# Optimization experiments

Hardware: AMD Instinct MI355X
Metric: run time of the kernel (lower is better)

The kernel has to match this reference:

```python
import jax, jax.numpy as jnp
import numpy as np

N_NODES = 100000
N_EDGES = 1200000
IN_DIM = 64
HID = 64
OUT = 10
N_GRAPHS = 256


def setup_inputs() -> dict:
    key = jax.random.key(0)
    ks = jax.random.split(key, 10)
    x = jax.random.normal(ks[0], (N_NODES, IN_DIM), dtype=jnp.float32)
    edge_index = jax.random.randint(ks[1], (2, N_EDGES), 0, N_NODES, dtype=jnp.int64)
    batch = jnp.sort(jax.random.randint(ks[2], (N_NODES,), 0, N_GRAPHS, dtype=jnp.int64))
    # GCNConv weights (glorot) and biases, final linear
    def glorot(k, fan_in, fan_out):
        s = jnp.sqrt(6.0 / (fan_in + fan_out)).astype(jnp.float32)
        return jax.random.uniform(k, (fan_in, fan_out), jnp.float32, -s, s)
    W1 = glorot(ks[3], IN_DIM, HID)
    b1 = jnp.zeros((HID,), jnp.float32)
    W2 = glorot(ks[4], HID, HID)
    b2 = jnp.zeros((HID,), jnp.float32)
    Wl = glorot(ks[5], HID, OUT)
    bl = jnp.zeros((OUT,), jnp.float32)
    return {"x": x, "edge_index": edge_index, "batch": batch,
            "W1": W1, "b1": b1, "W2": W2, "b2": b2, "Wl": Wl, "bl": bl}


def _gcn_conv(x, W, b, src, dst, n):
    # PyG GCNConv: add self-loops, symmetric deg^-1/2 normalization,
    # transform then aggregate, plus bias.
    h = x @ W  # [N, F_out]
    loop = jnp.arange(n, dtype=src.dtype)
    src_f = jnp.concatenate([src, loop])
    dst_f = jnp.concatenate([dst, loop])
    deg = jax.ops.segment_sum(jnp.ones_like(dst_f, dtype=h.dtype), dst_f, num_segments=n)
    dinv = jax.lax.rsqrt(jnp.maximum(deg, 1.0))  # self-loops guarantee deg>=1
    norm = dinv[src_f] * dinv[dst_f]  # [E+N]
    msgs = h[src_f] * norm[:, None]   # gather + scale (memory-bound)
    agg = jax.ops.segment_sum(msgs, dst_f, num_segments=n)
    return agg + b


def reference(x, edge_index, batch, W1, b1, W2, b2, Wl, bl):
    n = x.shape[0]
    src, dst = edge_index[0], edge_index[1]
    h = jax.nn.relu(_gcn_conv(x, W1, b1, src, dst, n))
    h = jax.nn.relu(_gcn_conv(h, W2, b2, src, dst, n))
    # global_mean_pool over batch vector
    sums = jax.ops.segment_sum(h, batch, num_segments=N_GRAPHS)
    cnt = jax.ops.segment_sum(jnp.ones((n,), h.dtype), batch, num_segments=N_GRAPHS)
    pooled = sums / jnp.maximum(cnt, 1.0)[:, None]  # [G, HID]
    return pooled @ Wl + bl  # [G, OUT]
```

## Files before the change

kernel.cpp:

```cpp
#include <hip/hip_runtime.h>
#include <hip/hip_bf16.h>


#define NFEAT 64
#define CAP 40

__device__ __forceinline__ float bf2f(__hip_bfloat16 h) { return __bfloat162float(h); }

__global__ __launch_bounds__(256) void dinv_kernel(const int* __restrict__ cursor,
                                                   float* __restrict__ dinv, int n) {
    int i = blockIdx.x * blockDim.x + threadIdx.x;
    if (i < n) dinv[i] = rsqrtf((float)(cursor[i] + 1));
}

__device__ __forceinline__ void gemm_rows(const float* __restrict__ in,
                                          __hip_bfloat16* __restrict__ out,
                                          int nRows, int rowBlock,
                                          float* wl, float* xrow) {
    const int tid = threadIdx.x;
    const int lane = tid & 63;
    const int w = tid >> 6;
    const int base = rowBlock * 64 + w * 16;
    for (int i = 0; i < 16; i++) {
        int r = base + i;
        if (r >= nRows) break;
        xrow[w * 64 + lane] = in[(size_t)r * NFEAT + lane];
        float acc = 0.f;
        const float4* x4 = (const float4*)(xrow + w * 64);
        #pragma unroll
        for (int kk = 0; kk < 16; kk++) {
            float4 xv = x4[kk];
            acc = fmaf(xv.x, wl[(kk * 4 + 0) * 64 + lane], acc);
            acc = fmaf(xv.y, wl[(kk * 4 + 1) * 64 + lane], acc);
            acc = fmaf(xv.z, wl[(kk * 4 + 2) * 64 + lane], acc);
            acc = fmaf(xv.w, wl[(kk * 4 + 3) * 64 + lane], acc);
        }
        out[(size_t)r * NFEAT + lane] = __float2bfloat16(acc);
    }
}

__global__ __launch_bounds__(256) void scatter_gemm1(
        const float* __restrict__ x, const float* __restrict__ W1,
        __hip_bfloat16* __restrict__ hbuf, int nN,
        const int* __restrict__ src, const int* __restrict__ dst,
        int* __restrict__ cursor, int* __restrict__ pad, int nE,
        int nGemmBlk, int edgesPerRank, int rng) {
    __shared__ float wl[64 * 64];
    __shared__ float xrow[4 * 64];
    const int b = blockIdx.x;
    if (b < nGemmBlk) {
        const int tid = threadIdx.x;
        #pragma unroll
        for (int i = 0; i < 16; i++) wl[tid + i * 256] = W1[tid + i * 256];
        __syncthreads();
        gemm_rows(x, hbuf, nN, b, wl, xrow);
    } else {
        const int xcd = b & 7;
        const int rank = (b - nGemmBlk) >> 3;
        const int lo = xcd * rng;
        int e0 = rank * edgesPerRank;
        int e1 = e0 + edgesPerRank; if (e1 > nE) e1 = nE;
        for (int e = e0 + threadIdx.x; e < e1; e += 256) {
            int d = dst[e];
            if ((unsigned)(d - lo) < (unsigned)rng) {
                int pos = atomicAdd(&cursor[d], 1);
                if (pos < CAP) pad[(size_t)d * CAP + pos] = src[e];
            }
        }
    }
}

__device__ __forceinline__ float agg_node(const __hip_bfloat16* __restrict__ hs,
                                          const float* __restrict__ dinv,
                                          const int* __restrict__ cursor,
                                          const int* __restrict__ pad,
                                          int n, int lane) {
    int cnt = cursor[n];
    cnt = cnt < CAP ? cnt : CAP;
    const float dn = dinv[n];
    const int* row = pad + (size_t)n * CAP;
    float acc = bf2f(hs[(size_t)n * NFEAT + lane]) * dn;
    int i = 0;
    for (; i + 3 < cnt; i += 4) {
        int s0 = row[i], s1 = row[i + 1], s2 = row[i + 2], s3 = row[i + 3];
        float d0 = dinv[s0], d1 = dinv[s1], d2 = dinv[s2], d3 = dinv[s3];
        float v0 = bf2f(hs[(size_t)s0 * NFEAT + lane]);
        float v1 = bf2f(hs[(size_t)s1 * NFEAT + lane]);
        float v2 = bf2f(hs[(size_t)s2 * NFEAT + lane]);
        float v3 = bf2f(hs[(size_t)s3 * NFEAT + lane]);
        acc = fmaf(v0, d0, acc); acc = fmaf(v1, d1, acc);
        acc = fmaf(v2, d2, acc); acc = fmaf(v3, d3, acc);
    }
    for (; i < cnt; ++i) {
        int s = row[i];
        acc = fmaf(bf2f(hs[(size_t)s * NFEAT + lane]), dinv[s], acc);
    }
    return acc * dn;
}

__global__ __launch_bounds__(256) void aggL1_gemm2(
        const __hip_bfloat16* __restrict__ hs1, const float* __restrict__ dinv,
        const int* __restrict__ cursor, const int* __restrict__ pad,
        const float* __restrict__ W2, const float* __restrict__ b1,
        __hip_bfloat16* __restrict__ hs2, int nN) {
    __shared__ float wl[64 * 64];
    __shared__ float xrow[4 * 64];
    const int tid = threadIdx.x;
    const int lane = tid & 63;
    const int w = tid >> 6;
    #pragma unroll
    for (int i = 0; i < 16; i++) wl[tid + i * 256] = W2[tid + i * 256];
    const float blane = b1[lane];
    __syncthreads();

    const int base = blockIdx.x * 16 + w * 4;
    #pragma unroll
    for (int i = 0; i < 4; i++) {
        int n = base + i;
        if (n >= nN) break;
        float a = agg_node(hs1, dinv, cursor, pad, n, lane);
        xrow[w * 64 + lane] = fmaxf(a + blane, 0.f);
        float acc = 0.f;
        const float4* x4 = (const float4*)(xrow + w * 64);
        #pragma unroll
        for (int kk = 0; kk < 16; kk++) {
            float4 xv = x4[kk];
            acc = fmaf(xv.x, wl[(kk * 4 + 0) * 64 + lane], acc);
            acc = fmaf(xv.y, wl[(kk * 4 + 1) * 64 + lane], acc);
            acc = fmaf(xv.z, wl[(kk * 4 + 2) * 64 + lane], acc);
            acc = fmaf(xv.w, wl[(kk * 4 + 3) * 64 + lane], acc);
        }
        hs2[(size_t)n * NFEAT + lane] = __float2bfloat16(acc);
    }
}

__global__ __launch_bounds__(256) void aggL2_pool(
        const __hip_bfloat16* __restrict__ hs2, const float* __restrict__ dinv,
        const int* __restrict__ cursor, const int* __restrict__ pad,
        const float* __restrict__ b2, const int* __restrict__ batch,
        float* __restrict__ psum, int nN) {
    const int lane = threadIdx.x & 63;
    const int w = threadIdx.x >> 6;
    const int n0 = (blockIdx.x * 4 + w) * 4;
    if (n0 >= nN) return;
    const int nEnd = (n0 + 4 < nN) ? n0 + 4 : nN;
    const float b = b2[lane];
    int gprev = batch[n0];
    float pacc = 0.f;
    for (int n = n0; n < nEnd; ++n) {
        int g = batch[n];
        if (g != gprev) {
            unsafeAtomicAdd(&psum[(size_t)gprev * NFEAT + lane], pacc);
            pacc = 0.f;
            gprev = g;
        }
        float a = agg_node(hs2, dinv, cursor, pad, n, lane);
        pacc += fmaxf(a + b, 0.f);
    }
    unsafeAtomicAdd(&psum[(size_t)gprev * NFEAT + lane], pacc);
}

__global__ __launch_bounds__(64) void final_kernel(const float* __restrict__ psum,
                                                   const int* __restrict__ batch, int nN,
                                                   const float* __restrict__ Wl,
                                                   const float* __restrict__ bl,
                                                   float* __restrict__ out) {
    const int g = blockIdx.x;
    const int j = threadIdx.x;
    int lo = 0, hi = nN;
    while (lo < hi) { int mid = (lo + hi) >> 1; if (batch[mid] < g) lo = mid + 1; else hi = mid; }
    const int start = lo;
    hi = nN;
    while (lo < hi) { int mid = (lo + hi) >> 1; if (batch[mid] < g + 1) lo = mid + 1; else hi = mid; }
    const int cnt = lo - start;
    __shared__ float p[64];
    p[j] = psum[g * 64 + j] / (float)(cnt > 1 ? cnt : 1);
    __syncthreads();
    if (j < 10) {
        float acc = bl[j];
        #pragma unroll
        for (int f = 0; f < 64; f++) acc = fmaf(p[f], Wl[f * 10 + j], acc);
        out[g * 10 + j] = acc;
    }
}

static inline size_t align256(size_t s) { return (s + 255) & ~(size_t)255; }

extern "C" void kernel_launch(void* const* d_in, const int* in_sizes, int n_in,
                              void* d_out, int out_size, void* d_ws, size_t ws_size,
                              hipStream_t stream) {
    const float* x     = (const float*)d_in[0];
    const int*   ei    = (const int*)d_in[1];
    const int*   batch = (const int*)d_in[2];
    const float* W1    = (const float*)d_in[3];
    const float* b1    = (const float*)d_in[4];
    const float* W2    = (const float*)d_in[5];
    const float* b2    = (const float*)d_in[6];
    const float* Wl    = (const float*)d_in[7];
    const float* bl    = (const float*)d_in[8];
    float* out = (float*)d_out;

    const int nN = in_sizes[0] / NFEAT;
    const int nE = in_sizes[1] / 2;
    const int nG = 256;
    const int* src = ei;
    const int* dst = ei + nE;

    char* w = (char*)d_ws;
    float* dinv   = (float*)w; w += align256((size_t)nN * 4);
    int*   cursor = (int*)w;   w += align256((size_t)nN * 4);
    int*   pad    = (int*)w;   w += align256((size_t)nN * CAP * 4);
    __hip_bfloat16* hs1 = (__hip_bfloat16*)w; w += align256((size_t)nN * NFEAT * 2);
    __hip_bfloat16* hs2 = (__hip_bfloat16*)w; w += align256((size_t)nN * NFEAT * 2);
    float* psum   = (float*)w; w += align256((size_t)nG * NFEAT * 4);

    const int nBlkN   = (nN + 255) / 256;
    const int nBlkRow = (nN + 63) / 64;
    const int nBlkAgg = (nN + 15) / 16;
    const int nGemmBlk = (nBlkRow + 7) & ~7;
    const int ranksPerXcd = 586;
    const int nScatBlk = ranksPerXcd * 8;
    const int edgesPerRank = (nE + ranksPerXcd - 1) / ranksPerXcd;
    const int rng = (nN + 7) / 8;

    (void)hipMemsetAsync(cursor, 0, (size_t)nN * 4, stream);
    (void)hipMemsetAsync(psum, 0, (size_t)nG * NFEAT * 4, stream);

    scatter_gemm1<<<nGemmBlk + nScatBlk, 256, 0, stream>>>(
        x, W1, hs1, nN, src, dst, cursor, pad, nE, nGemmBlk, edgesPerRank, rng);
    dinv_kernel<<<nBlkN, 256, 0, stream>>>(cursor, dinv, nN);

    aggL1_gemm2<<<nBlkAgg, 256, 0, stream>>>(hs1, dinv, cursor, pad, W2, b1, hs2, nN);

    aggL2_pool<<<nBlkAgg, 256, 0, stream>>>(hs2, dinv, cursor, pad, b2, batch, psum, nN);

    final_kernel<<<nG, 64, 0, stream>>>(psum, batch, nN, Wl, bl, out);
}
```

Baseline: 221.1 us.

## Prescale features by dinv, gather bf16 pairs with half-wave edge split

Replaces the separate dinv kernel with a pass that computes dinv and pre-multiplies the layer-1 bf16 features by the source node's dinv. Layer 2 features are likewise scaled at store time, so the aggregation loops need no per-neighbor dinv gathers. Each lane now loads two packed bf16 values, and the two half-waves split the neighbor list between them before being combined with a shuffle. The scatter stage also moves from 8 destination ranges to 4. Pre-scaling adds an extra read-modify-write pass over hs1 and rounds the scaled values to bf16 a second time.

Result: no change. 221.4 us (+0.2%).

```diff
diff --git a/kernel.cpp b/kernel.cpp
--- a/kernel.cpp
+++ b/kernel.cpp
@@ -5,13 +5,10 @@
 #define NFEAT 64
 #define CAP 40
 
-__device__ __forceinline__ float bf2f(__hip_bfloat16 h) { return __bfloat162float(h); }
-
-__global__ __launch_bounds__(256) void dinv_kernel(const int* __restrict__ cursor,
-                                                   float* __restrict__ dinv, int n) {
-    int i = blockIdx.x * blockDim.x + threadIdx.x;
-    if (i < n) dinv[i] = rsqrtf((float)(cursor[i] + 1));
-}
+typedef unsigned int uint;
+
+__device__ __forceinline__ float bflo(uint v) { return __uint_as_float(v << 16); }
+__device__ __forceinline__ float bfhi(uint v) { return __uint_as_float(v & 0xffff0000u); }
 
 __device__ __forceinline__ void gemm_rows(const float* __restrict__ in,
                                           __hip_bfloat16* __restrict__ out,
@@ -55,9 +52,9 @@
         __syncthreads();
         gemm_rows(x, hbuf, nN, b, wl, xrow);
     } else {
-        const int xcd = b & 7;
-        const int rank = (b - nGemmBlk) >> 3;
-        const int lo = xcd * rng;
+        const int range = (b & 7) >> 1;
+        const int rank = ((b - nGemmBlk) >> 3) * 2 + (b & 1);
+        const int lo = range * rng;
         int e0 = rank * edgesPerRank;
         int e1 = e0 + edgesPerRank; if (e1 > nE) e1 = nE;
         for (int e = e0 + threadIdx.x; e < e1; e += 256) {
@@ -70,36 +67,63 @@
     }
 }
 
-__device__ __forceinline__ float agg_node(const __hip_bfloat16* __restrict__ hs,
-                                          const float* __restrict__ dinv,
-                                          const int* __restrict__ cursor,
-                                          const int* __restrict__ pad,
-                                          int n, int lane) {
+__global__ __launch_bounds__(256) void scale_hs1(const int* __restrict__ cursor,
+                                                 float* __restrict__ dinv,
+                                                 uint* __restrict__ hs1u, int nN) {
+    int j = blockIdx.x * 256 + threadIdx.x;
+    if (j >= nN * 32) return;
+    int n = j >> 5;
+    float d = rsqrtf((float)(cursor[n] + 1));
+    if ((j & 31) == 0) dinv[n] = d;
+    uint v = hs1u[j];
+    float lo = bflo(v) * d, hi = bfhi(v) * d;
+    unsigned short l16 = __builtin_bit_cast(unsigned short, __float2bfloat16(lo));
+    unsigned short h16 = __builtin_bit_cast(unsigned short, __float2bfloat16(hi));
+    hs1u[j] = ((uint)h16 << 16) | (uint)l16;
+}
+
+__device__ __forceinline__ float2 agg_node_hw(const uint* __restrict__ hsu,
+                                              const int* __restrict__ cursor,
+                                              const int* __restrict__ pad,
+                                              int n, int tid) {
+    const int half = (tid >> 5) & 1;
+    const int fl = tid & 31;
     int cnt = cursor[n];
     cnt = cnt < CAP ? cnt : CAP;
-    const float dn = dinv[n];
     const int* row = pad + (size_t)n * CAP;
-    float acc = bf2f(hs[(size_t)n * NFEAT + lane]) * dn;
+    uint sv = hsu[(size_t)n * 32 + fl];
+    const float ws = half ? 0.f : 1.f;
+    float2 acc;
+    acc.x = bflo(sv) * ws;
+    acc.y = bfhi(sv) * ws;
     int i = 0;
-    for (; i + 3 < cnt; i += 4) {
-        int s0 = row[i], s1 = row[i + 1], s2 = row[i + 2], s3 = row[i + 3];
-        float d0 = dinv[s0], d1 = dinv[s1], d2 = dinv[s2], d3 = dinv[s3];
-        float v0 = bf2f(hs[(size_t)s0 * NFEAT + lane]);
-        float v1 = bf2f(hs[(size_t)s1 * NFEAT + lane]);
-        float v2 = bf2f(hs[(size_t)s2 * NFEAT + lane]);
-        float v3 = bf2f(hs[(size_t)s3 * NFEAT + lane]);
-        acc = fmaf(v0, d0, acc); acc = fmaf(v1, d1, acc);
-        acc = fmaf(v2, d2, acc); acc = fmaf(v3, d3, acc);
-    }
-    for (; i < cnt; ++i) {
-        int s = row[i];
-        acc = fmaf(bf2f(hs[(size_t)s * NFEAT + lane]), dinv[s], acc);
-    }
-    return acc * dn;
+    for (; i + 7 < cnt; i += 8) {
+        int s0 = row[i + half],     s1 = row[i + 2 + half];
+        int s2 = row[i + 4 + half], s3 = row[i + 6 + half];
+        uint v0 = hsu[(size_t)s0 * 32 + fl];
+        uint v1 = hsu[(size_t)s1 * 32 + fl];
+        uint v2 = hsu[(size_t)s2 * 32 + fl];
+        uint v3 = hsu[(size_t)s3 * 32 + fl];
+        acc.x += bflo(v0); acc.y += bfhi(v0);
+        acc.x += bflo(v1); acc.y += bfhi(v1);
+        acc.x += bflo(v2); acc.y += bfhi(v2);
+        acc.x += bflo(v3); acc.y += bfhi(v3);
+    }
+    for (; i < cnt; i += 2) {
+        int e = i + half;
+        int s = row[(e < cnt) ? e : i];
+        float wv = (e < cnt) ? 1.f : 0.f;
+        uint v = hsu[(size_t)s * 32 + fl];
+        acc.x = fmaf(bflo(v), wv, acc.x);
+        acc.y = fmaf(bfhi(v), wv, acc.y);
+    }
+    acc.x += __shfl_xor(acc.x, 32);
+    acc.y += __shfl_xor(acc.y, 32);
+    return acc;
 }
 
 __global__ __launch_bounds__(256) void aggL1_gemm2(
-        const __hip_bfloat16* __restrict__ hs1, const float* __restrict__ dinv,
+        const uint* __restrict__ hs1u, const float* __restrict__ dinv,
         const int* __restrict__ cursor, const int* __restrict__ pad,
         const float* __restrict__ W2, const float* __restrict__ b1,
         __hip_bfloat16* __restrict__ hs2, int nN) {
@@ -107,10 +131,10 @@
     __shared__ float xrow[4 * 64];
     const int tid = threadIdx.x;
     const int lane = tid & 63;
+    const int fl = tid & 31;
     const int w = tid >> 6;
     #pragma unroll
     for (int i = 0; i < 16; i++) wl[tid + i * 256] = W2[tid + i * 256];
-    const float blane = b1[lane];
     __syncthreads();
 
     const int base = blockIdx.x * 16 + w * 4;
@@ -118,8 +142,15 @@
     for (int i = 0; i < 4; i++) {
         int n = base + i;
         if (n >= nN) break;
-        float a = agg_node(hs1, dinv, cursor, pad, n, lane);
-        xrow[w * 64 + lane] = fmaxf(a + blane, 0.f);
+        float2 a = agg_node_hw(hs1u, cursor, pad, n, tid);
+        float dn = dinv[n];
+        if ((tid & 32) == 0) {
+            float2 bb = ((const float2*)b1)[fl];
+            float2 xr;
+            xr.x = fmaxf(fmaf(a.x, dn, bb.x), 0.f);
+            xr.y = fmaxf(fmaf(a.y, dn, bb.y), 0.f);
+            ((float2*)(xrow + w * 64))[fl] = xr;
+        }
         float acc = 0.f;
         const float4* x4 = (const float4*)(xrow + w * 64);
         #pragma unroll
@@ -130,34 +161,43 @@
             acc = fmaf(xv.z, wl[(kk * 4 + 2) * 64 + lane], acc);
             acc = fmaf(xv.w, wl[(kk * 4 + 3) * 64 + lane], acc);
         }
-        hs2[(size_t)n * NFEAT + lane] = __float2bfloat16(acc);
+        hs2[(size_t)n * NFEAT + lane] = __float2bfloat16(acc * dn);
     }
 }
 
 __global__ __launch_bounds__(256) void aggL2_pool(
-        const __hip_bfloat16* __restrict__ hs2, const float* __restrict__ dinv,
+        const uint* __restrict__ hs2u, const float* __restrict__ dinv,
         const int* __restrict__ cursor, const int* __restrict__ pad,
         const float* __restrict__ b2, const int* __restrict__ batch,
         float* __restrict__ psum, int nN) {
-    const int lane = threadIdx.x & 63;
-    const int w = threadIdx.x >> 6;
+    const int tid = threadIdx.x;
+    const int fl = tid & 31;
+    const int w = tid >> 6;
     const int n0 = (blockIdx.x * 4 + w) * 4;
     if (n0 >= nN) return;
     const int nEnd = (n0 + 4 < nN) ? n0 + 4 : nN;
-    const float b = b2[lane];
+    const float2 bb = ((const float2*)b2)[fl];
     int gprev = batch[n0];
-    float pacc = 0.f;
+    float2 pacc; pacc.x = 0.f; pacc.y = 0.f;
     for (int n = n0; n < nEnd; ++n) {
         int g = batch[n];
         if (g != gprev) {
-            unsafeAtomicAdd(&psum[(size_t)gprev * NFEAT + lane], pacc);
-            pacc = 0.f;
+            if ((tid & 32) == 0) {
+                unsafeAtomicAdd(&psum[(size_t)gprev * NFEAT + 2 * fl], pacc.x);
+                unsafeAtomicAdd(&psum[(size_t)gprev * NFEAT + 2 * fl + 1], pacc.y);
+            }
+            pacc.x = 0.f; pacc.y = 0.f;
             gprev = g;
         }
-        float a = agg_node(hs2, dinv, cursor, pad, n, lane);
-        pacc += fmaxf(a + b, 0.f);
-    }
-    unsafeAtomicAdd(&psum[(size_t)gprev * NFEAT + lane], pacc);
+        float2 a = agg_node_hw(hs2u, cursor, pad, n, tid);
+        float dn = dinv[n];
+        pacc.x += fmaxf(fmaf(a.x, dn, bb.x), 0.f);
+        pacc.y += fmaxf(fmaf(a.y, dn, bb.y), 0.f);
+    }
+    if ((tid & 32) == 0) {
+        unsafeAtomicAdd(&psum[(size_t)gprev * NFEAT + 2 * fl], pacc.x);
+        unsafeAtomicAdd(&psum[(size_t)gprev * NFEAT + 2 * fl + 1], pacc.y);
+    }
 }
 
 __global__ __launch_bounds__(64) void final_kernel(const float* __restrict__ psum,
@@ -214,25 +254,29 @@
     __hip_bfloat16* hs2 = (__hip_bfloat16*)w; w += align256((size_t)nN * NFEAT * 2);
     float* psum   = (float*)w; w += align256((size_t)nG * NFEAT * 4);
 
-    const int nBlkN   = (nN + 255) / 256;
     const int nBlkRow = (nN + 63) / 64;
     const int nBlkAgg = (nN + 15) / 16;
+    const int nBlkScl = (nN * 32 + 255) / 256;
     const int nGemmBlk = (nBlkRow + 7) & ~7;
     const int ranksPerXcd = 586;
     const int nScatBlk = ranksPerXcd * 8;
-    const int edgesPerRank = (nE + ranksPerXcd - 1) / ranksPerXcd;
-    const int rng = (nN + 7) / 8;
+    const int ranksPerRange = ranksPerXcd * 2;
+    const int edgesPerRank = (nE + ranksPerRange - 1) / ranksPerRange;
+    const int rng = (nN + 3) / 4;
 
     (void)hipMemsetAsync(cursor, 0, (size_t)nN * 4, stream);
     (void)hipMemsetAsync(psum, 0, (size_t)nG * NFEAT * 4, stream);
 
     scatter_gemm1<<<nGemmBlk + nScatBlk, 256, 0, stream>>>(
         x, W1, hs1, nN, src, dst, cursor, pad, nE, nGemmBlk, edgesPerRank, rng);
-    dinv_kernel<<<nBlkN, 256, 0, stream>>>(cursor, dinv, nN);
-
-    aggL1_gemm2<<<nBlkAgg, 256, 0, stream>>>(hs1, dinv, cursor, pad, W2, b1, hs2, nN);
-
-    aggL2_pool<<<nBlkAgg, 256, 0, stream>>>(hs2, dinv, cursor, pad, b2, batch, psum, nN);
+
+    scale_hs1<<<nBlkScl, 256, 0, stream>>>(cursor, dinv, (uint*)hs1, nN);
+
+    aggL1_gemm2<<<nBlkAgg, 256, 0, stream>>>((const uint*)hs1, dinv, cursor, pad,
+                                             W2, b1, hs2, nN);
+
+    aggL2_pool<<<nBlkAgg, 256, 0, stream>>>((const uint*)hs2, dinv, cursor, pad,
+                                            b2, batch, psum, nN);
 
     final_kernel<<<nG, 64, 0, stream>>>(psum, batch, nN, Wl, bl, out);
 }
```
